# Kernel tuning notes

Measured on AMD Instinct MI355X. Metric: run time of the kernel, lower is better.

Reference implementation:

```python
import jax, jax.numpy as jnp
import numpy as np

NUM_CLASSES = 60
FEATURE_DIM = 256
SEQ_LEN = 128
NUM_HEADS = 8
TOP_M = 20  # min(20, seq_len)
NUM_LAYERS = 2
EPS = 1e-5


def _layernorm(x, g, b):
    m = x.mean(-1, keepdims=True)
    v = ((x - m) ** 2).mean(-1, keepdims=True)
    return (x - m) * jax.lax.rsqrt(v + EPS) * g + b


def _topm_attention(x, qkv_w, qkv_b, proj_w, proj_b):
    # x: (B, N, C). Weights stored as (in, out) so y = x @ W + b.
    B, N, C = x.shape
    hd = C // NUM_HEADS
    scale = hd ** -0.5
    qkv = (x @ qkv_w + qkv_b).reshape(B, N, 3, NUM_HEADS, hd)
    q, k, v = (jnp.moveaxis(qkv[:, :, i], 2, 1) for i in range(3))  # (B,H,N,hd)
    s = jnp.einsum('bhnd,bhmd->bhnm', q, k) * scale  # (B,H,N,N)
    if TOP_M < N:
        # keep only per-query top-m scores (threshold at the m-th largest;
        # identical to torch scatter-mask for distinct float scores)
        kth = jax.lax.top_k(s, TOP_M)[0][..., -1:]
        s = jnp.where(s >= kth, s, -jnp.inf)
    a = jax.nn.softmax(s, axis=-1)  # dropout is identity in eval
    o = jnp.einsum('bhnm,bhmd->bhnd', a, v)
    o = o.transpose(0, 2, 1, 3).reshape(B, N, C)
    return o @ proj_w + proj_b


def setup_inputs() -> dict:
    key = jax.random.key(0)
    ks = jax.random.split(key, 20)
    B = 8 * NUM_CLASSES
    C = FEATURE_DIM
    d = {
        'reweighted_features': jax.random.normal(ks[0], (B, C, SEQ_LEN), jnp.float32),
        'pos_embed': jax.random.normal(ks[1], (1, SEQ_LEN, C), jnp.float32) * 0.02,
        'cls_w1': jax.random.normal(ks[2], (C, C // 2), jnp.float32) / np.sqrt(C),
        'cls_b1': jnp.zeros((C // 2,), jnp.float32),
        'cls_w2': jax.random.normal(ks[3], (C // 2, 1), jnp.float32) / np.sqrt(C // 2),
        'cls_b2': jnp.zeros((1,), jnp.float32),
    }
    for i in range(NUM_LAYERS):
        d[f'qkv_w{i}'] = jax.random.normal(ks[4 + 4 * i], (C, 3 * C), jnp.float32) / np.sqrt(C)
        d[f'qkv_b{i}'] = jnp.zeros((3 * C,), jnp.float32)
        d[f'proj_w{i}'] = jax.random.normal(ks[5 + 4 * i], (C, C), jnp.float32) / np.sqrt(C)
        d[f'proj_b{i}'] = jnp.zeros((C,), jnp.float32)
        d[f'ln_g{i}'] = jnp.ones((C,), jnp.float32)
        d[f'ln_b{i}'] = jnp.zeros((C,), jnp.float32)
    return d


def reference(reweighted_features, pos_embed, cls_w1, cls_b1, cls_w2, cls_b2,
              qkv_w0, qkv_b0, proj_w0, proj_b0, ln_g0, ln_b0,
              qkv_w1, qkv_b1, proj_w1, proj_b1, ln_g1, ln_b1):
    B = reweighted_features.shape[0] // NUM_CLASSES
    x = reweighted_features.transpose(0, 2, 1)  # (B*cls, N, C)
    x = x + pos_embed
    layers = [(qkv_w0, qkv_b0, proj_w0, proj_b0, ln_g0, ln_b0),
              (qkv_w1, qkv_b1, proj_w1, proj_b1, ln_g1, ln_b1)]
    for qw, qb, pw, pb, g, b in layers:
        x = _layernorm(x + _topm_attention(x, qw, qb, pw, pb), g, b)
    x = x.mean(axis=1)  # (B*cls, C)
    x = x.reshape(B, NUM_CLASSES, FEATURE_DIM)
    h = jax.nn.relu(x @ cls_w1 + cls_b1)  # dropout identity in eval
    logits = (h @ cls_w2 + cls_b2).reshape(B, NUM_CLASSES)
    return logits
```

## Files before the change

### kernel.cpp

```cpp
#include <hip/hip_runtime.h>
#include <hip/hip_bf16.h>
#include <cmath>

#define NSEQ 480
#define SEQN 128
#define CDIM 256
#define NH 8
#define HD 32
#define TOPM 20

typedef float f32x4 __attribute__((ext_vector_type(4)));
typedef short bf16x8 __attribute__((ext_vector_type(8)));

__device__ __forceinline__ unsigned short bf16_rn(float x) {
    unsigned int u = __float_as_uint(x);
    unsigned int r = (u + 0x7FFFu + ((u >> 16) & 1u)) >> 16;
    return (unsigned short)r;
}
__device__ __forceinline__ float bf16f(unsigned short h) {
    return __uint_as_float(((unsigned int)h) << 16);
}
__device__ __forceinline__ unsigned int okey(float v) {
    unsigned int u = __float_as_uint(v);
    return (u >> 31) ? ~u : (u | 0x80000000u);
}
__device__ __forceinline__ float okey_inv(unsigned int k) {
    return __uint_as_float((k >> 31) ? (k & 0x7FFFFFFFu) : ~k);
}
__device__ __forceinline__ unsigned pk_bf16(float a, float b) {
    union { __hip_bfloat162 h; unsigned u; } cv;
    cv.h = __float22bfloat162_rn(make_float2(a, b));
    return cv.u;
}
__device__ __forceinline__ void unpack_bf16x8(uint4 u, float* o) {
    o[0] = bf16f((unsigned short)(u.x & 0xffffu)); o[1] = bf16f((unsigned short)(u.x >> 16));
    o[2] = bf16f((unsigned short)(u.y & 0xffffu)); o[3] = bf16f((unsigned short)(u.y >> 16));
    o[4] = bf16f((unsigned short)(u.z & 0xffffu)); o[5] = bf16f((unsigned short)(u.z >> 16));
    o[6] = bf16f((unsigned short)(u.w & 0xffffu)); o[7] = bf16f((unsigned short)(u.w >> 16));
}

__global__ __launch_bounds__(256) void prep_kernel(const float* __restrict__ RW,
                                                   const float* __restrict__ POS,
                                                   unsigned short* __restrict__ XH,
                                                   unsigned short* __restrict__ XL) {
    int b = blockIdx.x, n0 = blockIdx.y * 32, c0 = blockIdx.z * 32;
    __shared__ float tile[32][33];
    int tx = threadIdx.x & 31, ty = threadIdx.x >> 5;
#pragma unroll
    for (int jj = 0; jj < 4; ++jj) {
        int c = c0 + ty + 8 * jj;
        tile[ty + 8 * jj][tx] = RW[((size_t)b * CDIM + c) * SEQN + n0 + tx];
    }
    __syncthreads();
#pragma unroll
    for (int jj = 0; jj < 4; ++jj) {
        int n = n0 + ty + 8 * jj;
        int c = c0 + tx;
        float val = tile[tx][ty + 8 * jj] + POS[n * CDIM + c];
        unsigned short hi = bf16_rn(val);
        size_t idx = (size_t)b * SEQN * CDIM + n * CDIM + c;
        XH[idx] = hi;
        XL[idx] = bf16_rn(val - bf16f(hi));
    }
}

__global__ __launch_bounds__(256) void wsplit_kernel(const float* __restrict__ W,
                                                     unsigned short* __restrict__ WtHi,
                                                     unsigned short* __restrict__ WtLo,
                                                     int ncols) {
    int k0 = blockIdx.x * 32, j0 = blockIdx.y * 32;
    __shared__ float tile[32][33];
    int tx = threadIdx.x & 31, ty = threadIdx.x >> 5;
#pragma unroll
    for (int jj = 0; jj < 4; ++jj)
        tile[ty + 8 * jj][tx] = W[(size_t)(k0 + ty + 8 * jj) * ncols + j0 + tx];
    __syncthreads();
#pragma unroll
    for (int jj = 0; jj < 4; ++jj) {
        float v = tile[tx][ty + 8 * jj];
        unsigned short hi = bf16_rn(v);
        unsigned short lo = bf16_rn(v - bf16f(hi));
        size_t idx = (size_t)(j0 + ty + 8 * jj) * 256 + k0 + tx;
        WtHi[idx] = hi;
        WtLo[idx] = lo;
    }
}

__global__ __launch_bounds__(256, 4) void attn_kernel(
    const unsigned short* __restrict__ XHi, const unsigned short* __restrict__ XLo,
    unsigned short* __restrict__ OH, unsigned short* __restrict__ OL,
    const unsigned short* __restrict__ WtHi, const unsigned short* __restrict__ WtLo,
    const float* __restrict__ BIAS) {
    const int bid = blockIdx.x;
    const int h = (bid >> 3) & 7;
    const int b = ((bid >> 6) << 3) | (bid & 7);
    const float scale = 0.17677669529663687f;

    __shared__ unsigned short qh[SEQN * HD], ql[SEQN * HD];
    __shared__ unsigned short kh[SEQN * HD], kl[SEQN * HD];
    __shared__ unsigned short vh[HD * SEQN];

    const int tid = threadIdx.x;
    const int w = tid >> 6;
    const int l = tid & 63;
    const int l15 = l & 15;
    const int sct = l >> 4;
    const size_t xbase = (size_t)b * SEQN * CDIM;

    f32x4 acc[2][6];
#pragma unroll
    for (int mi = 0; mi < 2; ++mi)
#pragma unroll
        for (int ni = 0; ni < 6; ++ni) acc[mi][ni] = (f32x4){0.f, 0.f, 0.f, 0.f};

#pragma unroll 2
    for (int ks = 0; ks < 8; ++ks) {
        const int kb = ks * 32;
        bf16x8 ahi[2], alo[2];
#pragma unroll
        for (int mi = 0; mi < 2; ++mi) {
            int row = w * 32 + mi * 16 + l15;
            size_t off = xbase + row * CDIM + kb + sct * 8;
            ahi[mi] = *reinterpret_cast<const bf16x8*>(XHi + off);
            alo[mi] = *reinterpret_cast<const bf16x8*>(XLo + off);
        }
#pragma unroll
        for (int ni = 0; ni < 6; ++ni) {
            int j = ((ni >> 1) << 8) + h * HD + ((ni & 1) << 4) + l15;
            const int woff = j * 256 + kb + sct * 8;
            bf16x8 bh = *reinterpret_cast<const bf16x8*>(WtHi + woff);
            if (ni < 4) {
                bf16x8 bl = *reinterpret_cast<const bf16x8*>(WtLo + woff);
#pragma unroll
                for (int mi = 0; mi < 2; ++mi) {
                    acc[mi][ni] = __builtin_amdgcn_mfma_f32_16x16x32_bf16(ahi[mi], bh, acc[mi][ni], 0, 0, 0);
                    acc[mi][ni] = __builtin_amdgcn_mfma_f32_16x16x32_bf16(ahi[mi], bl, acc[mi][ni], 0, 0, 0);
                    acc[mi][ni] = __builtin_amdgcn_mfma_f32_16x16x32_bf16(alo[mi], bh, acc[mi][ni], 0, 0, 0);
                }
            } else {
#pragma unroll
                for (int mi = 0; mi < 2; ++mi)
                    acc[mi][ni] = __builtin_amdgcn_mfma_f32_16x16x32_bf16(ahi[mi], bh, acc[mi][ni], 0, 0, 0);
            }
        }
    }
#pragma unroll
    for (int ni = 0; ni < 6; ++ni) {
        const int sel = ni >> 1;
        const int dcol = ((ni & 1) << 4) + l15;
        const float bias = BIAS[(sel << 8) + h * HD + dcol];
#pragma unroll
        for (int mi = 0; mi < 2; ++mi) {
            const int tb = w * 32 + mi * 16 + sct * 4;
            if (sel == 2) {
                float v0 = acc[mi][ni][0] + bias, v1 = acc[mi][ni][1] + bias;
                float v2 = acc[mi][ni][2] + bias, v3 = acc[mi][ni][3] + bias;
                unsigned pA = pk_bf16(v0, v1), pB = pk_bf16(v2, v3);
                int c0i = tb ^ ((dcol & 7) << 3);
                *reinterpret_cast<uint2*>(&vh[dcol * SEQN + c0i]) = make_uint2(pA, pB);
            } else {
                unsigned short* ph = sel ? kh : qh;
                unsigned short* pl = sel ? kl : ql;
#pragma unroll
                for (int r = 0; r < 4; ++r) {
                    float v = acc[mi][ni][r] + bias;
                    if (sel == 0) v *= scale;
                    unsigned short hi = bf16_rn(v);
                    int token = tb + r;
                    int idx = token * HD + (dcol ^ (((token >> 1) & 3) << 3));
                    ph[idx] = hi;
                    pl[idx] = bf16_rn(v - bf16f(hi));
                }
            }
        }
    }
    __syncthreads();

    f32x4 sacc[8][2];
#pragma unroll
    for (int mi = 0; mi < 8; ++mi)
#pragma unroll
        for (int ni = 0; ni < 2; ++ni) sacc[mi][ni] = (f32x4){0.f, 0.f, 0.f, 0.f};

    bf16x8 qfh[2], qfl[2];
#pragma unroll
    for (int ni = 0; ni < 2; ++ni) {
        int qrow = w * 32 + (ni << 4) + l15;
        int off = qrow * HD + ((sct * 8) ^ (((qrow >> 1) & 3) << 3));
        qfh[ni] = *reinterpret_cast<const bf16x8*>(qh + off);
        qfl[ni] = *reinterpret_cast<const bf16x8*>(ql + off);
    }
#pragma unroll
    for (int mi = 0; mi < 8; ++mi) {
        int krow = (mi << 4) + l15;
        int off = krow * HD + ((sct * 8) ^ (((krow >> 1) & 3) << 3));
        bf16x8 kfh = *reinterpret_cast<const bf16x8*>(kh + off);
        bf16x8 kfl = *reinterpret_cast<const bf16x8*>(kl + off);
#pragma unroll
        for (int ni = 0; ni < 2; ++ni) {
            sacc[mi][ni] = __builtin_amdgcn_mfma_f32_16x16x32_bf16(kfh, qfh[ni], sacc[mi][ni], 0, 0, 0);
            sacc[mi][ni] = __builtin_amdgcn_mfma_f32_16x16x32_bf16(kfh, qfl[ni], sacc[mi][ni], 0, 0, 0);
            sacc[mi][ni] = __builtin_amdgcn_mfma_f32_16x16x32_bf16(kfl, qfh[ni], sacc[mi][ni], 0, 0, 0);
        }
    }
#pragma unroll
    for (int mi = 0; mi < 8; ++mi)
#pragma unroll
        for (int ni = 0; ni < 2; ++ni)
#pragma unroll
            for (int r = 0; r < 4; ++r)
                sacc[mi][ni][r] = __uint_as_float(okey(sacc[mi][ni][r]));

    unsigned int km0 = 0u, km1 = 0u;
#pragma unroll
    for (int mi = 0; mi < 8; ++mi)
#pragma unroll
        for (int r = 0; r < 4; ++r) {
            km0 = max(km0, __float_as_uint(sacc[mi][0][r]));
            km1 = max(km1, __float_as_uint(sacc[mi][1][r]));
        }
    km0 = max(km0, (unsigned int)__shfl_xor((int)km0, 16));
    km0 = max(km0, (unsigned int)__shfl_xor((int)km0, 32));
    km1 = max(km1, (unsigned int)__shfl_xor((int)km1, 16));
    km1 = max(km1, (unsigned int)__shfl_xor((int)km1, 32));
    float mx0 = okey_inv(km0), mx1 = okey_inv(km1);

    unsigned p0, p1;
    {
        unsigned lo0 = 0u, hi0 = km0 + 1u, lo1 = 0u, hi1 = km1 + 1u;
        unsigned th0 = km0, th1 = km1;
        int dn0 = 0, dn1 = 0;
#pragma unroll 1
        for (int it = 0; it < 34; ++it) {
            if (__all(dn0 & dn1)) break;
            unsigned mid0 = lo0 + ((hi0 - lo0) >> 1);
            unsigned mid1 = lo1 + ((hi1 - lo1) >> 1);
            int c0 = 0, c1 = 0;
#pragma unroll
            for (int mi = 0; mi < 8; ++mi)
#pragma unroll
                for (int r = 0; r < 4; ++r) {
                    c0 += (__float_as_uint(sacc[mi][0][r]) >= mid0) ? 1 : 0;
                    c1 += (__float_as_uint(sacc[mi][1][r]) >= mid1) ? 1 : 0;
                }
            int mpk = c0 | (c1 << 8);
            mpk += __shfl_xor(mpk, 16);
            mpk += __shfl_xor(mpk, 32);
            c0 = mpk & 255;
            c1 = mpk >> 8;
            if (!dn0) {
                if (c0 == TOPM) { th0 = mid0; dn0 = 1; }
                else if (hi0 - lo0 <= 1u) { th0 = lo0; dn0 = 1; }
                else if (c0 > TOPM) lo0 = mid0;
                else hi0 = mid0;
            }
            if (!dn1) {
                if (c1 == TOPM) { th1 = mid1; dn1 = 1; }
                else if (hi1 - lo1 <= 1u) { th1 = lo1; dn1 = 1; }
                else if (c1 > TOPM) lo1 = mid1;
                else hi1 = mid1;
            }
        }
        p0 = th0; p1 = th1;
    }

    float s0 = 0.f, s1 = 0.f;
#pragma unroll
    for (int mi = 0; mi < 8; ++mi)
#pragma unroll
        for (int r = 0; r < 4; ++r) {
            unsigned int u0 = __float_as_uint(sacc[mi][0][r]);
            unsigned int u1 = __float_as_uint(sacc[mi][1][r]);
            float e0 = (u0 >= p0) ? __expf(okey_inv(u0) - mx0) : 0.f;
            float e1 = (u1 >= p1) ? __expf(okey_inv(u1) - mx1) : 0.f;
            sacc[mi][0][r] = e0;
            sacc[mi][1][r] = e1;
            s0 += e0;
            s1 += e1;
        }
    s0 += __shfl_xor(s0, 16);
    s0 += __shfl_xor(s0, 32);
    s1 += __shfl_xor(s1, 16);
    s1 += __shfl_xor(s1, 32);
    float i0 = 1.f / s0, i1 = 1.f / s1;

    unsigned w16[8][2][2];
#pragma unroll
    for (int mi = 0; mi < 8; ++mi)
#pragma unroll
        for (int ni = 0; ni < 2; ++ni)
#pragma unroll
            for (int p = 0; p < 2; ++p)
                w16[mi][ni][p] = pk_bf16(sacc[mi][ni][2 * p], sacc[mi][ni][2 * p + 1]);

    f32x4 oacc[2][2];
#pragma unroll
    for (int mi = 0; mi < 2; ++mi)
#pragma unroll
        for (int ni = 0; ni < 2; ++ni) oacc[mi][ni] = (f32x4){0.f, 0.f, 0.f, 0.f};

#pragma unroll
    for (int k = 0; k < 4; ++k) {
        bf16x8 bvh[2];
#pragma unroll
        for (int nio = 0; nio < 2; ++nio) {
            int drow = (nio << 4) + l15;
            int off = drow * SEQN + ((k * 32 + sct * 8) ^ ((drow & 7) << 3));
            bvh[nio] = *reinterpret_cast<const bf16x8*>(vh + off);
        }
#pragma unroll
        for (int mio = 0; mio < 2; ++mio) {
            union { unsigned u[4]; bf16x8 v8; } aw;
#pragma unroll
            for (int j = 0; j < 4; ++j) {
                int src = l15 + ((sct & 1) << 5) + ((j >> 1) << 4);
                unsigned a0 = (unsigned)__shfl((int)w16[2 * k][mio][j & 1], src);
                unsigned a1 = (unsigned)__shfl((int)w16[2 * k + 1][mio][j & 1], src);
                aw.u[j] = (sct >= 2) ? a1 : a0;
            }
#pragma unroll
            for (int nio = 0; nio < 2; ++nio)
                oacc[mio][nio] = __builtin_amdgcn_mfma_f32_16x16x32_bf16(aw.v8, bvh[nio], oacc[mio][nio], 0, 0, 0);
        }
    }
    float invO[2][4];
#pragma unroll
    for (int mio = 0; mio < 2; ++mio)
#pragma unroll
        for (int r = 0; r < 4; ++r)
            invO[mio][r] = __shfl(mio ? i1 : i0, sct * 4 + r);
#pragma unroll
    for (int mio = 0; mio < 2; ++mio)
#pragma unroll
        for (int nio = 0; nio < 2; ++nio)
#pragma unroll
            for (int r = 0; r < 4; ++r) {
                int token = w * 32 + mio * 16 + sct * 4 + r;
                int d = (nio << 4) + l15;
                size_t idx = ((size_t)b * SEQN + token) * CDIM + h * HD + d;
                float v = oacc[mio][nio][r] * invO[mio][r];
                unsigned short hi = bf16_rn(v);
                OH[idx] = hi;
                OL[idx] = bf16_rn(v - bf16f(hi));
            }
}

__global__ __launch_bounds__(256, 4) void projln_kernel(
    const unsigned short* __restrict__ OHp, const unsigned short* __restrict__ OLp,
    unsigned short* __restrict__ XH, unsigned short* __restrict__ XL,
    const unsigned short* __restrict__ W2H, const unsigned short* __restrict__ W2L,
    const float* __restrict__ PB, const float* __restrict__ G,
    const float* __restrict__ BB) {
    const int b = blockIdx.x;
    const int t0 = blockIdx.y * 32;
    __shared__ float vals[32 * 289];
    __shared__ float part[8][32][2];

    const int tid = threadIdx.x;
    const int w = tid >> 6;
    const int l = tid & 63;
    const int l15 = l & 15;
    const int sct = l >> 4;

    f32x4 acc[2][4];
#pragma unroll
    for (int mi = 0; mi < 2; ++mi)
#pragma unroll
        for (int ni = 0; ni < 4; ++ni) acc[mi][ni] = (f32x4){0.f, 0.f, 0.f, 0.f};

    const size_t obase = ((size_t)b * SEQN + t0) * CDIM;
#pragma unroll 2
    for (int ks = 0; ks < 8; ++ks) {
        const int kb = ks * 32;
        bf16x8 ahi[2], alo[2];
#pragma unroll
        for (int mi = 0; mi < 2; ++mi) {
            size_t off = obase + (size_t)(mi * 16 + l15) * CDIM + kb + sct * 8;
            ahi[mi] = *reinterpret_cast<const bf16x8*>(OHp + off);
            alo[mi] = *reinterpret_cast<const bf16x8*>(OLp + off);
        }
#pragma unroll
        for (int ni = 0; ni < 4; ++ni) {
            int j = w * 64 + ni * 16 + l15;
            int woff = j * 256 + kb + sct * 8;
            bf16x8 bh = *reinterpret_cast<const bf16x8*>(W2H + woff);
            bf16x8 bl = *reinterpret_cast<const bf16x8*>(W2L + woff);
#pragma unroll
            for (int mi = 0; mi < 2; ++mi) {
                acc[mi][ni] = __builtin_amdgcn_mfma_f32_16x16x32_bf16(ahi[mi], bh, acc[mi][ni], 0, 0, 0);
                acc[mi][ni] = __builtin_amdgcn_mfma_f32_16x16x32_bf16(ahi[mi], bl, acc[mi][ni], 0, 0, 0);
                acc[mi][ni] = __builtin_amdgcn_mfma_f32_16x16x32_bf16(alo[mi], bh, acc[mi][ni], 0, 0, 0);
            }
        }
    }
#pragma unroll
    for (int ni = 0; ni < 4; ++ni) {
        int j = w * 64 + ni * 16 + l15;
        float bias = PB[j];
#pragma unroll
        for (int mi = 0; mi < 2; ++mi)
#pragma unroll
            for (int r = 0; r < 4; ++r) {
                int tok = mi * 16 + sct * 4 + r;
                vals[tok * 289 + j] = acc[mi][ni][r] + bias;
            }
    }
    __syncthreads();

    const int row = tid & 31;
    const int cc = tid >> 5;
    const size_t rbase = ((size_t)b * SEQN + t0 + row) * CDIM + cc * 32;
    float v[32];
    {
        float ps = 0.f, pq = 0.f;
#pragma unroll
        for (int q = 0; q < 4; ++q) {
            uint4 hb = *reinterpret_cast<const uint4*>(XH + rbase + q * 8);
            uint4 lb = *reinterpret_cast<const uint4*>(XL + rbase + q * 8);
            float rh[8], rl[8];
            unpack_bf16x8(hb, rh);
            unpack_bf16x8(lb, rl);
#pragma unroll
            for (int jj = 0; jj < 8; ++jj) {
                int col = cc * 32 + q * 8 + jj;
                float val = vals[row * 289 + col] + rh[jj] + rl[jj];
                v[q * 8 + jj] = val;
                ps += val;
                pq = fmaf(val, val, pq);
            }
        }
        part[cc][row][0] = ps;
        part[cc][row][1] = pq;
    }
    __syncthreads();
    float s1 = 0.f, s2 = 0.f;
#pragma unroll
    for (int k = 0; k < 8; ++k) { s1 += part[k][row][0]; s2 += part[k][row][1]; }
    float m = s1 * (1.f / 256.f);
    float var = s2 * (1.f / 256.f) - m * m;
    float rstd = rsqrtf(var + 1e-5f);
#pragma unroll
    for (int q = 0; q < 4; ++q) {
        int col0 = cc * 32 + q * 8;
        float4 g0 = *reinterpret_cast<const float4*>(G + col0);
        float4 g1 = *reinterpret_cast<const float4*>(G + col0 + 4);
        float4 b0 = *reinterpret_cast<const float4*>(BB + col0);
        float4 b1 = *reinterpret_cast<const float4*>(BB + col0 + 4);
        float gg[8] = {g0.x, g0.y, g0.z, g0.w, g1.x, g1.y, g1.z, g1.w};
        float bb2[8] = {b0.x, b0.y, b0.z, b0.w, b1.x, b1.y, b1.z, b1.w};
        unsigned hw[4], lw[4];
#pragma unroll
        for (int p2 = 0; p2 < 4; ++p2) {
            float y0 = (v[q * 8 + p2 * 2] - m) * rstd * gg[p2 * 2] + bb2[p2 * 2];
            float y1 = (v[q * 8 + p2 * 2 + 1] - m) * rstd * gg[p2 * 2 + 1] + bb2[p2 * 2 + 1];
            unsigned short h0 = bf16_rn(y0), h1 = bf16_rn(y1);
            unsigned short lo0 = bf16_rn(y0 - bf16f(h0)), lo1 = bf16_rn(y1 - bf16f(h1));
            hw[p2] = (unsigned)h0 | ((unsigned)h1 << 16);
            lw[p2] = (unsigned)lo0 | ((unsigned)lo1 << 16);
        }
        *reinterpret_cast<uint4*>(XH + rbase + q * 8) = make_uint4(hw[0], hw[1], hw[2], hw[3]);
        *reinterpret_cast<uint4*>(XL + rbase + q * 8) = make_uint4(lw[0], lw[1], lw[2], lw[3]);
    }
}

__global__ __launch_bounds__(256) void cls_kernel(const unsigned short* __restrict__ XH,
                                                  const unsigned short* __restrict__ XL,
                                                  const float* __restrict__ W1,
                                                  const float* __restrict__ B1,
                                                  const float* __restrict__ W2,
                                                  const float* __restrict__ B2,
                                                  float* __restrict__ OUT) {
    int b = blockIdx.x;
    __shared__ float xm[256];
    __shared__ float hred[128];
    int tid = threadIdx.x;
    float sm = 0.f;
    for (int n = 0; n < SEQN; ++n) {
        size_t idx = ((size_t)b * SEQN + n) * CDIM + tid;
        sm += bf16f(XH[idx]) + bf16f(XL[idx]);
    }
    xm[tid] = sm * (1.f / 128.f);
    __syncthreads();
    if (tid < 128) {
        float a = B1[tid];
        for (int k = 0; k < CDIM; ++k) a = fmaf(xm[k], W1[k * 128 + tid], a);
        a = fmaxf(a, 0.f);
        hred[tid] = a * W2[tid];
    }
    __syncthreads();
    for (int off = 64; off > 0; off >>= 1) {
        if (tid < off) hred[tid] += hred[tid + off];
        __syncthreads();
    }
    if (tid == 0) OUT[b] = hred[0] + B2[0];
}

extern "C" void kernel_launch(void* const* d_in, const int* in_sizes, int n_in,
                              void* d_out, int out_size, void* d_ws, size_t ws_size,
                              hipStream_t stream) {
    const float* RW  = (const float*)d_in[0];
    const float* POS = (const float*)d_in[1];
    const float* CW1 = (const float*)d_in[2];
    const float* CB1 = (const float*)d_in[3];
    const float* CW2 = (const float*)d_in[4];
    const float* CB2 = (const float*)d_in[5];

    const size_t NTOK = (size_t)NSEQ * SEQN * CDIM;
    unsigned short* OH = (unsigned short*)d_ws;
    unsigned short* OL = OH + NTOK;
    unsigned short* XH = OL + NTOK;
    unsigned short* XL = XH + NTOK;
    unsigned short* WtHi = XL + NTOK;
    unsigned short* WtLo = WtHi + (size_t)768 * 256;
    unsigned short* W2H = WtLo + (size_t)768 * 256;
    unsigned short* W2L = W2H + (size_t)256 * 256;

    prep_kernel<<<dim3(NSEQ, 4, 8), 256, 0, stream>>>(RW, POS, XH, XL);

    for (int li = 0; li < 2; ++li) {
        const float* qw = (const float*)d_in[6 + 6 * li];
        const float* qb = (const float*)d_in[7 + 6 * li];
        const float* pw = (const float*)d_in[8 + 6 * li];
        const float* pb = (const float*)d_in[9 + 6 * li];
        const float* lg = (const float*)d_in[10 + 6 * li];
        const float* lb = (const float*)d_in[11 + 6 * li];
        wsplit_kernel<<<dim3(8, 24), 256, 0, stream>>>(qw, WtHi, WtLo, 768);
        wsplit_kernel<<<dim3(8, 8), 256, 0, stream>>>(pw, W2H, W2L, 256);
        attn_kernel<<<NSEQ * NH, 256, 0, stream>>>(XH, XL, OH, OL, WtHi, WtLo, qb);
        projln_kernel<<<dim3(NSEQ, 4), 256, 0, stream>>>(OH, OL, XH, XL, W2H, W2L, pb, lg, lb);
    }

    cls_kernel<<<NSEQ, 256, 0, stream>>>(XH, XL, CW1, CB1, CW2, CB2, (float*)d_out);
}
```

Baseline: 787.8 us.

## Vectorize prep stores, merge weight splits, tighten top-k search bounds, add setprio

The prep kernel now writes two packed bf16 values per 32-bit store instead of single 16-bit stores. The two weight-split launches per layer are merged into one kernel launch. The top-k binary search starts its lower bound at the per-row minimum key instead of zero, which should cut iterations. s_setprio hints are wrapped around the MFMA loops in the attention kernel to favour matrix issue across waves. These are several unrelated small tweaks, each with modest expected impact.

```diff
diff --git a/kernel.cpp b/kernel.cpp
--- a/kernel.cpp
+++ b/kernel.cpp
@@ -52,23 +52,34 @@
         tile[ty + 8 * jj][tx] = RW[((size_t)b * CDIM + c) * SEQN + n0 + tx];
     }
     __syncthreads();
-#pragma unroll
-    for (int jj = 0; jj < 4; ++jj) {
-        int n = n0 + ty + 8 * jj;
-        int c = c0 + tx;
-        float val = tile[tx][ty + 8 * jj] + POS[n * CDIM + c];
-        unsigned short hi = bf16_rn(val);
-        size_t idx = (size_t)b * SEQN * CDIM + n * CDIM + c;
-        XH[idx] = hi;
-        XL[idx] = bf16_rn(val - bf16f(hi));
-    }
-}
-
-__global__ __launch_bounds__(256) void wsplit_kernel(const float* __restrict__ W,
-                                                     unsigned short* __restrict__ WtHi,
-                                                     unsigned short* __restrict__ WtLo,
-                                                     int ncols) {
-    int k0 = blockIdx.x * 32, j0 = blockIdx.y * 32;
+    const int cp = threadIdx.x & 15;
+    const int nr = threadIdx.x >> 4;
+#pragma unroll
+    for (int pass = 0; pass < 2; ++pass) {
+        int n = n0 + nr + 16 * pass;
+        int c = c0 + cp * 2;
+        const float* prow = POS + (n - n0 + n0) * CDIM + c;
+        float v0 = tile[cp * 2 + 0][nr + 16 * pass] + prow[0];
+        float v1 = tile[cp * 2 + 1][nr + 16 * pass] + prow[1];
+        unsigned short h0 = bf16_rn(v0), h1 = bf16_rn(v1);
+        unsigned short l0 = bf16_rn(v0 - bf16f(h0)), l1 = bf16_rn(v1 - bf16f(h1));
+        size_t widx = ((size_t)b * SEQN * CDIM + (size_t)n * CDIM + c) >> 1;
+        reinterpret_cast<unsigned*>(XH)[widx] = (unsigned)h0 | ((unsigned)h1 << 16);
+        reinterpret_cast<unsigned*>(XL)[widx] = (unsigned)l0 | ((unsigned)l1 << 16);
+    }
+}
+
+__global__ __launch_bounds__(256) void wsplit2_kernel(
+    const float* __restrict__ Wq, const float* __restrict__ Wp,
+    unsigned short* __restrict__ QH, unsigned short* __restrict__ QL,
+    unsigned short* __restrict__ PH, unsigned short* __restrict__ PL) {
+    int k0 = blockIdx.x * 32;
+    int yy = blockIdx.y;
+    const float* W;
+    unsigned short *WH, *WL;
+    int ncols, j0;
+    if (yy < 24) { W = Wq; WH = QH; WL = QL; ncols = 768; j0 = yy * 32; }
+    else         { W = Wp; WH = PH; WL = PL; ncols = 256; j0 = (yy - 24) * 32; }
     __shared__ float tile[32][33];
     int tx = threadIdx.x & 31, ty = threadIdx.x >> 5;
 #pragma unroll
@@ -81,8 +92,8 @@
         unsigned short hi = bf16_rn(v);
         unsigned short lo = bf16_rn(v - bf16f(hi));
         size_t idx = (size_t)(j0 + ty + 8 * jj) * 256 + k0 + tx;
-        WtHi[idx] = hi;
-        WtLo[idx] = lo;
+        WH[idx] = hi;
+        WL[idx] = lo;
     }
 }
 
@@ -190,6 +201,7 @@
         qfh[ni] = *reinterpret_cast<const bf16x8*>(qh + off);
         qfl[ni] = *reinterpret_cast<const bf16x8*>(ql + off);
     }
+    __builtin_amdgcn_s_setprio(1);
 #pragma unroll
     for (int mi = 0; mi < 8; ++mi) {
         int krow = (mi << 4) + l15;
@@ -203,6 +215,7 @@
             sacc[mi][ni] = __builtin_amdgcn_mfma_f32_16x16x32_bf16(kfl, qfh[ni], sacc[mi][ni], 0, 0, 0);
         }
     }
+    __builtin_amdgcn_s_setprio(0);
 #pragma unroll
     for (int mi = 0; mi < 8; ++mi)
 #pragma unroll
@@ -211,23 +224,29 @@
             for (int r = 0; r < 4; ++r)
                 sacc[mi][ni][r] = __uint_as_float(okey(sacc[mi][ni][r]));
 
-    unsigned int km0 = 0u, km1 = 0u;
+    unsigned int km0 = 0u, km1 = 0u, kn0 = 0xFFFFFFFFu, kn1 = 0xFFFFFFFFu;
 #pragma unroll
     for (int mi = 0; mi < 8; ++mi)
 #pragma unroll
         for (int r = 0; r < 4; ++r) {
-            km0 = max(km0, __float_as_uint(sacc[mi][0][r]));
-            km1 = max(km1, __float_as_uint(sacc[mi][1][r]));
+            unsigned int u0 = __float_as_uint(sacc[mi][0][r]);
+            unsigned int u1 = __float_as_uint(sacc[mi][1][r]);
+            km0 = max(km0, u0); kn0 = min(kn0, u0);
+            km1 = max(km1, u1); kn1 = min(kn1, u1);
         }
     km0 = max(km0, (unsigned int)__shfl_xor((int)km0, 16));
     km0 = max(km0, (unsigned int)__shfl_xor((int)km0, 32));
     km1 = max(km1, (unsigned int)__shfl_xor((int)km1, 16));
     km1 = max(km1, (unsigned int)__shfl_xor((int)km1, 32));
+    kn0 = min(kn0, (unsigned int)__shfl_xor((int)kn0, 16));
+    kn0 = min(kn0, (unsigned int)__shfl_xor((int)kn0, 32));
+    kn1 = min(kn1, (unsigned int)__shfl_xor((int)kn1, 16));
+    kn1 = min(kn1, (unsigned int)__shfl_xor((int)kn1, 32));
     float mx0 = okey_inv(km0), mx1 = okey_inv(km1);
 
     unsigned p0, p1;
     {
-        unsigned lo0 = 0u, hi0 = km0 + 1u, lo1 = 0u, hi1 = km1 + 1u;
+        unsigned lo0 = kn0, hi0 = km0 + 1u, lo1 = kn1, hi1 = km1 + 1u;
         unsigned th0 = km0, th1 = km1;
         int dn0 = 0, dn1 = 0;
 #pragma unroll 1
@@ -318,9 +337,11 @@
                 unsigned a1 = (unsigned)__shfl((int)w16[2 * k + 1][mio][j & 1], src);
                 aw.u[j] = (sct >= 2) ? a1 : a0;
             }
+            __builtin_amdgcn_s_setprio(1);
 #pragma unroll
             for (int nio = 0; nio < 2; ++nio)
                 oacc[mio][nio] = __builtin_amdgcn_mfma_f32_16x16x32_bf16(aw.v8, bvh[nio], oacc[mio][nio], 0, 0, 0);
+            __builtin_amdgcn_s_setprio(0);
         }
     }
     float invO[2][4];
@@ -524,8 +545,7 @@
         const float* pb = (const float*)d_in[9 + 6 * li];
         const float* lg = (const float*)d_in[10 + 6 * li];
         const float* lb = (const float*)d_in[11 + 6 * li];
-        wsplit_kernel<<<dim3(8, 24), 256, 0, stream>>>(qw, WtHi, WtLo, 768);
-        wsplit_kernel<<<dim3(8, 8), 256, 0, stream>>>(pw, W2H, W2L, 256);
+        wsplit2_kernel<<<dim3(8, 32), 256, 0, stream>>>(qw, pw, WtHi, WtLo, W2H, W2L);
         attn_kernel<<<NSEQ * NH, 256, 0, stream>>>(XH, XL, OH, OL, WtHi, WtLo, qb);
         projln_kernel<<<dim3(NSEQ, 4), 256, 0, stream>>>(OH, OL, XH, XL, W2H, W2L, pb, lg, lb);
     }
```

New measurement: 784.7 us. Within noise of the previous version (-0.4%).
